# Kernel optimization log

Hardware: AMD Instinct MI355X
Metric: run time of the kernel (lower is better)

## Reference

```python
import jax, jax.numpy as jnp
import numpy as np

B, N, D = 8, 1024, 512
H = 8
DH = D // H
EPS_DIST = 1e-8
EPS_LN = 1e-5


def _layer_norm(x, gamma, beta):
    mu = jnp.mean(x, axis=-1, keepdims=True)
    var = jnp.mean((x - mu) ** 2, axis=-1, keepdims=True)
    return (x - mu) * jax.lax.rsqrt(var + EPS_LN) * gamma + beta


def setup_inputs() -> dict:
    key = jax.random.key(0)
    ks = jax.random.split(key, 6)
    scale = 1.0 / np.sqrt(D)
    inp = {
        "x": jax.random.normal(ks[0], (B, N, D), dtype=jnp.float32),
        "Wq": jax.random.normal(ks[1], (D, D), dtype=jnp.float32) * scale,
        "Wk": jax.random.normal(ks[2], (D, D), dtype=jnp.float32) * scale,
        "Wv": jax.random.normal(ks[3], (D, D), dtype=jnp.float32) * scale,
        "Wo": jax.random.normal(ks[4], (D, D), dtype=jnp.float32) * scale,
        "bq": jnp.zeros((D,), jnp.float32),
        "bk": jnp.zeros((D,), jnp.float32),
        "bv": jnp.zeros((D,), jnp.float32),
        "bo": jnp.zeros((D,), jnp.float32),
        "ln1_g": jnp.ones((D,), jnp.float32),
        "ln1_b": jnp.zeros((D,), jnp.float32),
        "ln2_g": jnp.ones((D,), jnp.float32),
        "ln2_b": jnp.zeros((D,), jnp.float32),
    }
    return inp


def reference(x, Wq, bq, Wk, bk, Wv, bv, Wo, bo, ln1_g, ln1_b, ln2_g, ln2_b):
    residual = x
    h = _layer_norm(x, ln1_g, ln1_b)  # pre-norm

    def heads(t):
        # [B,N,D] -> [B,H,N,DH]
        return t.reshape(B, N, H, DH).transpose(0, 2, 1, 3)

    q = heads(h @ Wq + bq)
    k = heads(h @ Wk + bk)
    v = heads(h @ Wv + bv)

    # Euclidean pairwise distance via ||q||^2 + ||k||^2 - 2 q.k expansion
    q_sq = jnp.sum(q * q, axis=-1)[..., :, None]      # [B,H,N,1]
    k_sq = jnp.sum(k * k, axis=-1)[..., None, :]      # [B,H,1,N]
    qk = jnp.einsum("bhnd,bhmd->bhnm", q, k)          # [B,H,N,N]
    d2 = jnp.maximum(q_sq + k_sq - 2.0 * qk, 0.0)
    dist = jnp.sqrt(d2 + EPS_DIST)

    # distance -> attention score: smaller distance = higher attention
    attn = jax.nn.softmax(-dist, axis=-1)             # [B,H,N,N]

    out = jnp.einsum("bhnm,bhmd->bhnd", attn, v)      # [B,H,N,DH]
    out = out.transpose(0, 2, 1, 3).reshape(B, N, D)
    out = out @ Wo + bo

    y = residual + out
    y = _layer_norm(y, ln2_g, ln2_b)
    return y
```

## Files before the change

kernel.cpp:

```cpp
#include <hip/hip_runtime.h>
#include <math.h>

typedef __attribute__((ext_vector_type(8))) short short8;
typedef __attribute__((ext_vector_type(4))) float f32x4;

constexpr int B  = 8;
constexpr int N  = 1024;
constexpr int D  = 512;
constexpr int H  = 8;
constexpr int DH = 64;
constexpr int M_ROWS = 8192;
constexpr float EPS_DIST = 1e-8f;
constexpr float EPS_LN   = 1e-5f;

__device__ inline unsigned short bfbits(float f) {
    union { float f; unsigned u; } v; v.f = f;
    unsigned r = v.u + 0x7fffu + ((v.u >> 16) & 1u);
    return (unsigned short)(r >> 16);
}
__device__ inline float bf2f(unsigned short s) {
    union { unsigned u; float f; } v; v.u = ((unsigned)s) << 16; return v.f;
}

__device__ inline void async_ld16(unsigned short* lds, const unsigned short* g) {
    __builtin_amdgcn_global_load_lds(
        (const __attribute__((address_space(1))) unsigned int*)(g),
        (__attribute__((address_space(3))) unsigned int*)(lds),
        16, 0, 0);
}

__global__ __launch_bounds__(256) void prep_kernel(const float* __restrict__ Wq,
                                                   const float* __restrict__ Wk,
                                                   const float* __restrict__ Wv,
                                                   const float* __restrict__ Wo,
                                                   unsigned short* __restrict__ WtAll,
                                                   const float* __restrict__ x,
                                                   const float* __restrict__ ln1_g,
                                                   const float* __restrict__ ln1_b,
                                                   unsigned short* __restrict__ h_bf) {
    const int bxg = blockIdx.x;
    if (bxg < 256) {
        int sub = bxg >> 6;
        const float* W = sub == 0 ? Wq : sub == 1 ? Wk : sub == 2 ? Wv : Wo;
        unsigned short* Wt = WtAll + (size_t)sub * 262144;
        int t = (bxg & 63) * 256 + threadIdx.x;
        int tn = t & 127, tk = t >> 7;
        int k = tk * 4, n = tn * 4;
        float4 r0 = *(const float4*)&W[(size_t)(k + 0) * 512 + n];
        float4 r1 = *(const float4*)&W[(size_t)(k + 1) * 512 + n];
        float4 r2 = *(const float4*)&W[(size_t)(k + 2) * 512 + n];
        float4 r3 = *(const float4*)&W[(size_t)(k + 3) * 512 + n];
        ushort4 c;
        c.x = bfbits(r0.x); c.y = bfbits(r1.x); c.z = bfbits(r2.x); c.w = bfbits(r3.x);
        *(ushort4*)&Wt[(size_t)(n + 0) * 512 + k] = c;
        c.x = bfbits(r0.y); c.y = bfbits(r1.y); c.z = bfbits(r2.y); c.w = bfbits(r3.y);
        *(ushort4*)&Wt[(size_t)(n + 1) * 512 + k] = c;
        c.x = bfbits(r0.z); c.y = bfbits(r1.z); c.z = bfbits(r2.z); c.w = bfbits(r3.z);
        *(ushort4*)&Wt[(size_t)(n + 2) * 512 + k] = c;
        c.x = bfbits(r0.w); c.y = bfbits(r1.w); c.z = bfbits(r2.w); c.w = bfbits(r3.w);
        *(ushort4*)&Wt[(size_t)(n + 3) * 512 + k] = c;
    } else {
        const int w = threadIdx.x >> 6, lane = threadIdx.x & 63;
        const int row = (bxg - 256) * 4 + w;
        const float4* xr = (const float4*)(x + (size_t)row * D);
        float4 a = xr[lane], b2 = xr[lane + 64];
        float s = a.x + a.y + a.z + a.w + b2.x + b2.y + b2.z + b2.w;
        #pragma unroll
        for (int o = 1; o < 64; o <<= 1) s += __shfl_xor(s, o, 64);
        const float mu = s * (1.0f / 512.0f);
        float d0 = a.x - mu, d1 = a.y - mu, d2 = a.z - mu, d3 = a.w - mu;
        float e0 = b2.x - mu, e1 = b2.y - mu, e2 = b2.z - mu, e3 = b2.w - mu;
        float vs = d0*d0 + d1*d1 + d2*d2 + d3*d3 + e0*e0 + e1*e1 + e2*e2 + e3*e3;
        #pragma unroll
        for (int o = 1; o < 64; o <<= 1) vs += __shfl_xor(vs, o, 64);
        const float rstd = rsqrtf(vs * (1.0f / 512.0f) + EPS_LN);
        const float4* g4 = (const float4*)ln1_g;
        const float4* b4 = (const float4*)ln1_b;
        float4 ga = g4[lane], gb = g4[lane + 64];
        float4 ba = b4[lane], bb = b4[lane + 64];
        ushort4 u;
        u.x = bfbits(d0 * rstd * ga.x + ba.x);
        u.y = bfbits(d1 * rstd * ga.y + ba.y);
        u.z = bfbits(d2 * rstd * ga.z + ba.z);
        u.w = bfbits(d3 * rstd * ga.w + ba.w);
        *(ushort4*)&h_bf[(size_t)row * 512 + lane * 4] = u;
        u.x = bfbits(e0 * rstd * gb.x + bb.x);
        u.y = bfbits(e1 * rstd * gb.y + bb.y);
        u.z = bfbits(e2 * rstd * gb.z + bb.z);
        u.w = bfbits(e3 * rstd * gb.w + bb.w);
        *(ushort4*)&h_bf[(size_t)row * 512 + 256 + lane * 4] = u;
    }
}

__global__ __launch_bounds__(256) void ln2_kernel(const unsigned short* __restrict__ y0,
                                                  const float* __restrict__ res,
                                                  const float* __restrict__ gamma,
                                                  const float* __restrict__ beta,
                                                  float* __restrict__ out) {
    const int w = threadIdx.x >> 6, lane = threadIdx.x & 63;
    const int row = blockIdx.x * 4 + w;
    const ushort4* y4 = (const ushort4*)(y0 + (size_t)row * D);
    const float4*  r4 = (const float4*)(res + (size_t)row * D);
    ushort4 ya = y4[lane], yb = y4[lane + 64];
    float4  ra = r4[lane], rb = r4[lane + 64];
    float v0 = bf2f(ya.x) + ra.x, v1 = bf2f(ya.y) + ra.y;
    float v2 = bf2f(ya.z) + ra.z, v3 = bf2f(ya.w) + ra.w;
    float v4 = bf2f(yb.x) + rb.x, v5 = bf2f(yb.y) + rb.y;
    float v6 = bf2f(yb.z) + rb.z, v7 = bf2f(yb.w) + rb.w;
    float s = v0 + v1 + v2 + v3 + v4 + v5 + v6 + v7;
    #pragma unroll
    for (int o = 1; o < 64; o <<= 1) s += __shfl_xor(s, o, 64);
    const float mu = s * (1.0f / 512.0f);
    v0 -= mu; v1 -= mu; v2 -= mu; v3 -= mu;
    v4 -= mu; v5 -= mu; v6 -= mu; v7 -= mu;
    float vs = v0*v0 + v1*v1 + v2*v2 + v3*v3 + v4*v4 + v5*v5 + v6*v6 + v7*v7;
    #pragma unroll
    for (int o = 1; o < 64; o <<= 1) vs += __shfl_xor(vs, o, 64);
    const float rstd = rsqrtf(vs * (1.0f / 512.0f) + EPS_LN);
    const float4* g4 = (const float4*)gamma;
    const float4* b4 = (const float4*)beta;
    float4 ga = g4[lane], gb = g4[lane + 64];
    float4 ba = b4[lane], bb = b4[lane + 64];
    float4 o1, o2;
    o1.x = v0 * rstd * ga.x + ba.x; o1.y = v1 * rstd * ga.y + ba.y;
    o1.z = v2 * rstd * ga.z + ba.z; o1.w = v3 * rstd * ga.w + ba.w;
    o2.x = v4 * rstd * gb.x + bb.x; o2.y = v5 * rstd * gb.y + bb.y;
    o2.z = v6 * rstd * gb.z + bb.z; o2.w = v7 * rstd * gb.w + bb.w;
    float4* orow = (float4*)(out + (size_t)row * D);
    orow[lane]      = o1;
    orow[lane + 64] = o2;
}

template <int MODE, int MT>
__global__ __launch_bounds__(256) void gemm128(const unsigned short* __restrict__ A,
                                               const unsigned short* __restrict__ Wt,
                                               const float* __restrict__ bias0,
                                               const float* __restrict__ bias1,
                                               const float* __restrict__ bias2,
                                               void* __restrict__ o0,
                                               unsigned short* __restrict__ Ko,
                                               unsigned short* __restrict__ Vo,
                                               float* __restrict__ sq0,
                                               float* __restrict__ sq1) {
    constexpr int RB = M_ROWS / MT;
    constexpr int NI = MT / 32;
    constexpr int ASZ = MT * 64, BSZ = 128 * 64;
    constexpr int SMSZ = (MODE == 1) ? ((ASZ + BSZ > 18432) ? ASZ + BSZ : 18432)
                                     : (ASZ + BSZ);
    __shared__ unsigned short smem[SMSZ];
    unsigned short* As = smem;
    unsigned short* Bs = smem + ASZ;

    const int id = blockIdx.x;
    const int by = id & (RB - 1), bx = id / RB;
    const int tid = threadIdx.x;
    const int lane = tid & 63, wv = tid >> 6;
    const int quad = lane >> 4, l15 = lane & 15;
    const int row0 = by * MT, col0 = bx * 128;
    const int wm = (wv & 1) * (MT / 2), wn = (wv >> 1) * 64;

    f32x4 acc[NI][4];
    #pragma unroll
    for (int i = 0; i < NI; ++i)
        #pragma unroll
        for (int j = 0; j < 4; ++j) acc[i][j] = (f32x4){0.f, 0.f, 0.f, 0.f};

    const unsigned short* Ag = A  + (size_t)row0 * 512;
    const unsigned short* Bg = Wt + (size_t)col0 * 512;

    for (int k0 = 0; k0 < 512; k0 += 64) {
        __syncthreads();
        #pragma unroll
        for (int c = 0; c < ASZ / 2048; ++c) {
            int fu = c * 2048 + tid * 8;
            int r = fu >> 6, ko = fu & 63;
            async_ld16(As + fu, Ag + (size_t)r * 512 + k0 + ko);
        }
        #pragma unroll
        for (int c = 0; c < BSZ / 2048; ++c) {
            int fu = c * 2048 + tid * 8;
            int r = fu >> 6, ko = fu & 63;
            async_ld16(Bs + fu, Bg + (size_t)r * 512 + k0 + ko);
        }
        __syncthreads();

        #pragma unroll
        for (int ks = 0; ks < 2; ++ks) {
            short8 af[NI], bf[4];
            #pragma unroll
            for (int i = 0; i < NI; ++i)
                af[i] = *(const short8*)&As[(wm + i * 16 + l15) * 64 + ks * 32 + quad * 8];
            #pragma unroll
            for (int j = 0; j < 4; ++j)
                bf[j] = *(const short8*)&Bs[(wn + j * 16 + l15) * 64 + ks * 32 + quad * 8];
            #pragma unroll
            for (int i = 0; i < NI; ++i)
                #pragma unroll
                for (int j = 0; j < 4; ++j)
                    acc[i][j] = __builtin_amdgcn_mfma_f32_16x16x32_bf16(af[i], bf[j], acc[i][j], 0, 0, 0);
        }
    }

    if (MODE == 0) {
        unsigned short* C = (unsigned short*)o0;
        #pragma unroll
        for (int i = 0; i < NI; ++i)
            #pragma unroll
            for (int j = 0; j < 4; ++j) {
                int col = col0 + wn + j * 16 + l15;
                float bv = bias0[col];
                #pragma unroll
                for (int r = 0; r < 4; ++r) {
                    int row = row0 + wm + i * 16 + quad * 4 + r;
                    C[(size_t)row * 512 + col] = bfbits(acc[i][j][r] + bv);
                }
            }
    } else {
        const int colg = col0 + wn;
        const int seg = colg >> 9;
        const int hh = (colg & 511) >> 6;
        const float* bias = seg == 0 ? bias0 : seg == 1 ? bias1 : bias2;

        if (seg < 2) {
            unsigned short* dst = seg == 0 ? (unsigned short*)o0 : Ko;
            float* sq = seg == 0 ? sq0 : sq1;
            #pragma unroll
            for (int i = 0; i < NI; ++i) {
                const int m0 = row0 + wm + i * 16 + quad * 4;
                float ss[4] = {0.f, 0.f, 0.f, 0.f};
                #pragma unroll
                for (int j = 0; j < 4; ++j) {
                    float bvj = bias[hh * 64 + j * 16 + l15];
                    #pragma unroll
                    for (int r = 0; r < 4; ++r) {
                        float v = acc[i][j][r] + bvj;
                        unsigned short ub = bfbits(v);
                        float vr = bf2f(ub);
                        ss[r] += vr * vr;
                        int m = m0 + r;
                        int b_ = m >> 10, n_ = m & 1023;
                        dst[((size_t)((b_ * 8 + hh) * 1024) + n_) * 64 + j * 16 + l15] = ub;
                    }
                }
                #pragma unroll
                for (int r = 0; r < 4; ++r) {
                    float s = ss[r];
                    s += __shfl_xor(s, 1, 64);
                    s += __shfl_xor(s, 2, 64);
                    s += __shfl_xor(s, 4, 64);
                    s += __shfl_xor(s, 8, 64);
                    if (l15 == 0) {
                        int m = m0 + r;
                        sq[(size_t)((m >> 10) * 8 + hh) * 1024 + (m & 1023)] = s;
                    }
                }
            }
        } else {
            __syncthreads();
            unsigned short* T = smem + wv * 4608;
            #pragma unroll
            for (int i = 0; i < NI; ++i)
                #pragma unroll
                for (int j = 0; j < 4; ++j) {
                    float bvj = bias[hh * 64 + j * 16 + l15];
                    ushort4 pk;
                    pk.x = bfbits(acc[i][j][0] + bvj);
                    pk.y = bfbits(acc[i][j][1] + bvj);
                    pk.z = bfbits(acc[i][j][2] + bvj);
                    pk.w = bfbits(acc[i][j][3] + bvj);
                    *(ushort4*)&T[(j * 16 + l15) * 72 + i * 16 + quad * 4] = pk;
                }
            const int b_ = (row0 + wm) >> 10;
            const int nbase = (row0 + wm) & 1023;
            unsigned short* Vg = Vo + ((size_t)((b_ * 8 + hh) * 64)) * 1024 + nbase;
            #pragma unroll
            for (int it = 0; it < 8; ++it) {
                int dl = it * 8 + (lane >> 3);
                int nl = (lane & 7) * 8;
                uint4 v = *(const uint4*)&T[dl * 72 + nl];
                *(uint4*)&Vg[(size_t)dl * 1024 + nl] = v;
            }
        }
    }
}

__global__ __launch_bounds__(256) void attn_kernel(const unsigned short* __restrict__ Q,
                                                   const unsigned short* __restrict__ K,
                                                   const unsigned short* __restrict__ Vt,
                                                   const float* __restrict__ qsq,
                                                   const float* __restrict__ ksq,
                                                   unsigned short* __restrict__ O) {
    __shared__ unsigned short Ks[2][64][72];
    __shared__ unsigned short Vs[2][64][72];
    __shared__ unsigned short Ps[4][32][72];
    __shared__ float ksq_s[2][64];

    const int id = blockIdx.x;
    const int bh = id & 63, qb = id >> 6;
    const int q0 = qb * 128;
    const int tid = threadIdx.x;
    const int lane = tid & 63, w = tid >> 6;
    const int quad = lane >> 4, l15 = lane & 15;
    const int b_ = bh >> 3, h_ = bh & 7;

    const unsigned short* Qb = Q  + (size_t)bh * N * DH;
    const unsigned short* Kb = K  + (size_t)bh * N * DH;
    const unsigned short* Vb = Vt + (size_t)bh * DH * N;

    short8 qf[2][2];
    #pragma unroll
    for (int qh = 0; qh < 2; ++qh) {
        const unsigned short* qp = Qb + (size_t)(q0 + w * 32 + qh * 16 + l15) * 64 + quad * 8;
        qf[qh][0] = *(const short8*)qp;
        qf[qh][1] = *(const short8*)(qp + 32);
    }
    float qe[2][4];
    #pragma unroll
    for (int qh = 0; qh < 2; ++qh)
        #pragma unroll
        for (int r = 0; r < 4; ++r)
            qe[qh][r] = qsq[bh * N + q0 + w * 32 + qh * 16 + quad * 4 + r] + EPS_DIST;

    f32x4 oacc[2][4];
    #pragma unroll
    for (int qh = 0; qh < 2; ++qh)
        #pragma unroll
        for (int dt = 0; dt < 4; ++dt) oacc[qh][dt] = (f32x4){0.f, 0.f, 0.f, 0.f};
    float dpart[2][4] = {};

    const int e0 = tid, e1 = tid + 256;
    const int r0s = e0 >> 3, c0s = (e0 & 7) * 8;
    const int r1s = e1 >> 3, c1s = (e1 & 7) * 8;
    uint4 kreg0, kreg1, vreg0, vreg1;
    float ksreg = 0.f;

    kreg0 = *(const uint4*)(Kb + (size_t)r0s * 64 + c0s);
    kreg1 = *(const uint4*)(Kb + (size_t)r1s * 64 + c1s);
    vreg0 = *(const uint4*)(Vb + (size_t)r0s * N + c0s);
    vreg1 = *(const uint4*)(Vb + (size_t)r1s * N + c1s);
    if (tid < 64) ksreg = ksq[bh * N + tid];

    *(uint4*)&Ks[0][r0s][c0s] = kreg0;
    *(uint4*)&Ks[0][r1s][c1s] = kreg1;
    *(uint4*)&Vs[0][r0s][c0s] = vreg0;
    *(uint4*)&Vs[0][r1s][c1s] = vreg1;
    if (tid < 64) ksq_s[0][tid] = ksreg;
    __syncthreads();

    for (int kt = 0; kt < 16; ++kt) {
        const int cur = kt & 1;
        if (kt < 15) {
            kreg0 = *(const uint4*)(Kb + (size_t)((kt + 1) * 64 + r0s) * 64 + c0s);
            kreg1 = *(const uint4*)(Kb + (size_t)((kt + 1) * 64 + r1s) * 64 + c1s);
            vreg0 = *(const uint4*)(Vb + (size_t)r0s * N + (kt + 1) * 64 + c0s);
            vreg1 = *(const uint4*)(Vb + (size_t)r1s * N + (kt + 1) * 64 + c1s);
            if (tid < 64) ksreg = ksq[bh * N + (kt + 1) * 64 + tid];
        }

        #pragma unroll
        for (int kb = 0; kb < 4; ++kb) {
            short8 kf0 = *(const short8*)&Ks[cur][kb * 16 + l15][quad * 8];
            short8 kf1 = *(const short8*)&Ks[cur][kb * 16 + l15][32 + quad * 8];
            float ks2 = ksq_s[cur][kb * 16 + l15];
            #pragma unroll
            for (int qh = 0; qh < 2; ++qh) {
                f32x4 sa = (f32x4){0.f, 0.f, 0.f, 0.f};
                sa = __builtin_amdgcn_mfma_f32_16x16x32_bf16(qf[qh][0], kf0, sa, 0, 0, 0);
                sa = __builtin_amdgcn_mfma_f32_16x16x32_bf16(qf[qh][1], kf1, sa, 0, 0, 0);
                #pragma unroll
                for (int r = 0; r < 4; ++r) {
                    float d2 = fmaf(-2.0f, sa[r], qe[qh][r] + ks2);
                    d2 = fmaxf(d2, EPS_DIST);
                    float p = __expf(-__builtin_amdgcn_sqrtf(d2));
                    dpart[qh][r] += p;
                    union { float f; unsigned u; } pu; pu.f = p;
                    Ps[w][qh * 16 + quad * 4 + r][kb * 16 + l15] = (unsigned short)(pu.u >> 16);
                }
            }
        }

        short8 vf[4][2];
        #pragma unroll
        for (int dt = 0; dt < 4; ++dt)
            #pragma unroll
            for (int kc = 0; kc < 2; ++kc)
                vf[dt][kc] = *(const short8*)&Vs[cur][dt * 16 + l15][kc * 32 + quad * 8];
        #pragma unroll
        for (int kc = 0; kc < 2; ++kc) {
            short8 pf0 = *(const short8*)&Ps[w][l15][kc * 32 + quad * 8];
            short8 pf1 = *(const short8*)&Ps[w][16 + l15][kc * 32 + quad * 8];
            #pragma unroll
            for (int dt = 0; dt < 4; ++dt) {
                oacc[0][dt] = __builtin_amdgcn_mfma_f32_16x16x32_bf16(pf0, vf[dt][kc], oacc[0][dt], 0, 0, 0);
                oacc[1][dt] = __builtin_amdgcn_mfma_f32_16x16x32_bf16(pf1, vf[dt][kc], oacc[1][dt], 0, 0, 0);
            }
        }

        if (kt < 15) {
            *(uint4*)&Ks[cur ^ 1][r0s][c0s] = kreg0;
            *(uint4*)&Ks[cur ^ 1][r1s][c1s] = kreg1;
            *(uint4*)&Vs[cur ^ 1][r0s][c0s] = vreg0;
            *(uint4*)&Vs[cur ^ 1][r1s][c1s] = vreg1;
            if (tid < 64) ksq_s[cur ^ 1][tid] = ksreg;
        }
        __syncthreads();
    }

    float rinv[2][4];
    #pragma unroll
    for (int qh = 0; qh < 2; ++qh)
        #pragma unroll
        for (int r = 0; r < 4; ++r) {
            float s = dpart[qh][r];
            s += __shfl_xor(s, 1, 64);
            s += __shfl_xor(s, 2, 64);
            s += __shfl_xor(s, 4, 64);
            s += __shfl_xor(s, 8, 64);
            rinv[qh][r] = __builtin_amdgcn_rcpf(s);
        }

    #pragma unroll
    for (int qh = 0; qh < 2; ++qh)
        #pragma unroll
        for (int dt = 0; dt < 4; ++dt)
            #pragma unroll
            for (int r = 0; r < 4; ++r) {
                int n_ = q0 + w * 32 + qh * 16 + quad * 4 + r;
                O[((size_t)(b_ * N + n_) * D) + h_ * DH + dt * 16 + l15] =
                    bfbits(oacc[qh][dt][r] * rinv[qh][r]);
            }
}

extern "C" void kernel_launch(void* const* d_in, const int* in_sizes, int n_in,
                              void* d_out, int out_size, void* d_ws, size_t ws_size,
                              hipStream_t stream) {
    const float* x     = (const float*)d_in[0];
    const float* Wq    = (const float*)d_in[1];
    const float* Wk    = (const float*)d_in[2];
    const float* Wv    = (const float*)d_in[3];
    const float* Wo    = (const float*)d_in[4];
    const float* bq    = (const float*)d_in[5];
    const float* bk    = (const float*)d_in[6];
    const float* bv    = (const float*)d_in[7];
    const float* bo    = (const float*)d_in[8];
    const float* ln1_g = (const float*)d_in[9];
    const float* ln1_b = (const float*)d_in[10];
    const float* ln2_g = (const float*)d_in[11];
    const float* ln2_b = (const float*)d_in[12];
    float* out = (float*)d_out;

    unsigned short* WtAll = (unsigned short*)d_ws;
    unsigned short* h_bf  = WtAll + 4 * 262144;
    unsigned short* Qb    = h_bf + 4194304;
    unsigned short* Kb    = Qb + 4194304;
    unsigned short* Vtg   = Kb + 4194304;
    unsigned short* Ob    = Vtg + 4194304;
    unsigned short* Y0    = Ob + 4194304;
    float* qsq = (float*)(Y0 + 4194304);
    float* ksq = qsq + 65536;

    prep_kernel<<<256 + M_ROWS / 4, 256, 0, stream>>>(Wq, Wk, Wv, Wo, WtAll,
                                                      x, ln1_g, ln1_b, h_bf);

    gemm128<1, 128><<<768, 256, 0, stream>>>(h_bf, WtAll, bq, bk, bv,
                                             Qb, Kb, Vtg, qsq, ksq);

    attn_kernel<<<512, 256, 0, stream>>>(Qb, Kb, Vtg, qsq, ksq, Ob);

    gemm128<0, 64><<<512, 256, 0, stream>>>(Ob, WtAll + 3 * 262144, bo,
                                            nullptr, nullptr, Y0,
                                            nullptr, nullptr, nullptr, nullptr);

    ln2_kernel<<<M_ROWS / 4, 256, 0, stream>>>(Y0, x, ln2_g, ln2_b, out);
}
```

Baseline: 180.1 us.

## Keep attention probabilities in registers via permlane swaps and swizzle K/V LDS tiles

The attention kernel now computes the transposed score tile, with K as the A operand. Q fragments are pre-scaled by -2 through a bf16 bit trick, and the accumulator is seeded with ||q||^2+||k||^2, so the distance expansion folds into the MFMA. The bf16 probabilities are packed and redistributed across lanes with permlane32/permlane16 swaps. This replaces the round trip through the per-wave Ps LDS buffer and feeds the PV MFMAs directly. K/V LDS tiles drop their padding in favour of an XOR swizzle, and row normalizers are broadcast through a small LDS scratch. The change removes LDS traffic and bank conflicts, at the cost of more lane-permute work and a bit-hack scaling that treats zero and subnormal inputs slightly differently.

```diff
diff --git a/kernel.cpp b/kernel.cpp
--- a/kernel.cpp
+++ b/kernel.cpp
@@ -3,6 +3,7 @@
 
 typedef __attribute__((ext_vector_type(8))) short short8;
 typedef __attribute__((ext_vector_type(4))) float f32x4;
+typedef __attribute__((ext_vector_type(2))) unsigned uint2v;
 
 constexpr int B  = 8;
 constexpr int N  = 1024;
@@ -290,9 +291,8 @@
                                                    const float* __restrict__ qsq,
                                                    const float* __restrict__ ksq,
                                                    unsigned short* __restrict__ O) {
-    __shared__ unsigned short Ks[2][64][72];
-    __shared__ unsigned short Vs[2][64][72];
-    __shared__ unsigned short Ps[4][32][72];
+    __shared__ unsigned short Ks[2][64][64];
+    __shared__ unsigned short Vs[2][64][64];
     __shared__ float ksq_s[2][64];
 
     const int id = blockIdx.x;
@@ -313,111 +313,132 @@
         const unsigned short* qp = Qb + (size_t)(q0 + w * 32 + qh * 16 + l15) * 64 + quad * 8;
         qf[qh][0] = *(const short8*)qp;
         qf[qh][1] = *(const short8*)(qp + 32);
-    }
-    float qe[2][4];
+        unsigned* qw = (unsigned*)&qf[qh][0];
+        #pragma unroll
+        for (int j = 0; j < 8; ++j) qw[j] = (qw[j] ^ 0x80008000u) + 0x00800080u;
+    }
+    float qe[2];
+    qe[0] = qsq[bh * N + q0 + w * 32 + l15] + EPS_DIST;
+    qe[1] = qsq[bh * N + q0 + w * 32 + 16 + l15] + EPS_DIST;
+
+    f32x4 oacc[2][4];
     #pragma unroll
     for (int qh = 0; qh < 2; ++qh)
         #pragma unroll
-        for (int r = 0; r < 4; ++r)
-            qe[qh][r] = qsq[bh * N + q0 + w * 32 + qh * 16 + quad * 4 + r] + EPS_DIST;
-
-    f32x4 oacc[2][4];
-    #pragma unroll
-    for (int qh = 0; qh < 2; ++qh)
-        #pragma unroll
         for (int dt = 0; dt < 4; ++dt) oacc[qh][dt] = (f32x4){0.f, 0.f, 0.f, 0.f};
-    float dpart[2][4] = {};
-
-    const int e0 = tid, e1 = tid + 256;
-    const int r0s = e0 >> 3, c0s = (e0 & 7) * 8;
-    const int r1s = e1 >> 3, c1s = (e1 & 7) * 8;
+    float dsum[2] = {0.f, 0.f};
+
+    const int r0s = tid >> 3, r1s = r0s + 32;
+    const int cbase = (tid & 7) * 8;
+    const int csw = cbase ^ ((r0s & 7) << 3);
     uint4 kreg0, kreg1, vreg0, vreg1;
     float ksreg = 0.f;
 
-    kreg0 = *(const uint4*)(Kb + (size_t)r0s * 64 + c0s);
-    kreg1 = *(const uint4*)(Kb + (size_t)r1s * 64 + c1s);
-    vreg0 = *(const uint4*)(Vb + (size_t)r0s * N + c0s);
-    vreg1 = *(const uint4*)(Vb + (size_t)r1s * N + c1s);
+    kreg0 = *(const uint4*)(Kb + (size_t)r0s * 64 + cbase);
+    kreg1 = *(const uint4*)(Kb + (size_t)r1s * 64 + cbase);
+    vreg0 = *(const uint4*)(Vb + (size_t)r0s * N + cbase);
+    vreg1 = *(const uint4*)(Vb + (size_t)r1s * N + cbase);
     if (tid < 64) ksreg = ksq[bh * N + tid];
 
-    *(uint4*)&Ks[0][r0s][c0s] = kreg0;
-    *(uint4*)&Ks[0][r1s][c1s] = kreg1;
-    *(uint4*)&Vs[0][r0s][c0s] = vreg0;
-    *(uint4*)&Vs[0][r1s][c1s] = vreg1;
+    *(uint4*)&Ks[0][r0s][csw] = kreg0;
+    *(uint4*)&Ks[0][r1s][csw] = kreg1;
+    *(uint4*)&Vs[0][r0s][csw] = vreg0;
+    *(uint4*)&Vs[0][r1s][csw] = vreg1;
     if (tid < 64) ksq_s[0][tid] = ksreg;
     __syncthreads();
 
     for (int kt = 0; kt < 16; ++kt) {
         const int cur = kt & 1;
         if (kt < 15) {
-            kreg0 = *(const uint4*)(Kb + (size_t)((kt + 1) * 64 + r0s) * 64 + c0s);
-            kreg1 = *(const uint4*)(Kb + (size_t)((kt + 1) * 64 + r1s) * 64 + c1s);
-            vreg0 = *(const uint4*)(Vb + (size_t)r0s * N + (kt + 1) * 64 + c0s);
-            vreg1 = *(const uint4*)(Vb + (size_t)r1s * N + (kt + 1) * 64 + c1s);
+            kreg0 = *(const uint4*)(Kb + (size_t)((kt + 1) * 64 + r0s) * 64 + cbase);
+            kreg1 = *(const uint4*)(Kb + (size_t)((kt + 1) * 64 + r1s) * 64 + cbase);
+            vreg0 = *(const uint4*)(Vb + (size_t)r0s * N + (kt + 1) * 64 + cbase);
+            vreg1 = *(const uint4*)(Vb + (size_t)r1s * N + (kt + 1) * 64 + cbase);
             if (tid < 64) ksreg = ksq[bh * N + (kt + 1) * 64 + tid];
         }
 
         #pragma unroll
-        for (int kb = 0; kb < 4; ++kb) {
-            short8 kf0 = *(const short8*)&Ks[cur][kb * 16 + l15][quad * 8];
-            short8 kf1 = *(const short8*)&Ks[cur][kb * 16 + l15][32 + quad * 8];
-            float ks2 = ksq_s[cur][kb * 16 + l15];
+        for (int kc = 0; kc < 2; ++kc) {
+            unsigned Wp[2][2][2];
+            #pragma unroll
+            for (int kh = 0; kh < 2; ++kh) {
+                const int kb = kc * 2 + kh;
+                const int krow = kb * 16 + l15;
+                const int ksw = (krow & 7) << 3;
+                short8 kf0 = *(const short8*)&Ks[cur][krow][(quad * 8) ^ ksw];
+                short8 kf1 = *(const short8*)&Ks[cur][krow][(32 + quad * 8) ^ ksw];
+                f32x4 ks2 = *(const f32x4*)&ksq_s[cur][kb * 16 + quad * 4];
+                #pragma unroll
+                for (int qh = 0; qh < 2; ++qh) {
+                    f32x4 sa;
+                    #pragma unroll
+                    for (int r = 0; r < 4; ++r) sa[r] = ks2[r] + qe[qh];
+                    sa = __builtin_amdgcn_mfma_f32_16x16x32_bf16(kf0, qf[qh][0], sa, 0, 0, 0);
+                    sa = __builtin_amdgcn_mfma_f32_16x16x32_bf16(kf1, qf[qh][1], sa, 0, 0, 0);
+                    float pr[4];
+                    #pragma unroll
+                    for (int r = 0; r < 4; ++r) {
+                        float d2 = fmaxf(sa[r], EPS_DIST);
+                        float p = __expf(-__builtin_amdgcn_sqrtf(d2));
+                        dsum[qh] += p;
+                        pr[r] = p;
+                    }
+                    union { float f; unsigned u; } u0, u1, u2, u3;
+                    u0.f = pr[0]; u1.f = pr[1]; u2.f = pr[2]; u3.f = pr[3];
+                    Wp[qh][kh][0] = (u1.u & 0xFFFF0000u) | (u0.u >> 16);
+                    Wp[qh][kh][1] = (u3.u & 0xFFFF0000u) | (u2.u >> 16);
+                }
+            }
+
+            short8 vf[4];
+            #pragma unroll
+            for (int dt = 0; dt < 4; ++dt) {
+                const int vrow = dt * 16 + l15;
+                vf[dt] = *(const short8*)&Vs[cur][vrow][(kc * 32 + quad * 8) ^ ((vrow & 7) << 3)];
+            }
+
             #pragma unroll
             for (int qh = 0; qh < 2; ++qh) {
-                f32x4 sa = (f32x4){0.f, 0.f, 0.f, 0.f};
-                sa = __builtin_amdgcn_mfma_f32_16x16x32_bf16(qf[qh][0], kf0, sa, 0, 0, 0);
-                sa = __builtin_amdgcn_mfma_f32_16x16x32_bf16(qf[qh][1], kf1, sa, 0, 0, 0);
-                #pragma unroll
-                for (int r = 0; r < 4; ++r) {
-                    float d2 = fmaf(-2.0f, sa[r], qe[qh][r] + ks2);
-                    d2 = fmaxf(d2, EPS_DIST);
-                    float p = __expf(-__builtin_amdgcn_sqrtf(d2));
-                    dpart[qh][r] += p;
-                    union { float f; unsigned u; } pu; pu.f = p;
-                    Ps[w][qh * 16 + quad * 4 + r][kb * 16 + l15] = (unsigned short)(pu.u >> 16);
-                }
-            }
-        }
-
-        short8 vf[4][2];
-        #pragma unroll
-        for (int dt = 0; dt < 4; ++dt)
-            #pragma unroll
-            for (int kc = 0; kc < 2; ++kc)
-                vf[dt][kc] = *(const short8*)&Vs[cur][dt * 16 + l15][kc * 32 + quad * 8];
-        #pragma unroll
-        for (int kc = 0; kc < 2; ++kc) {
-            short8 pf0 = *(const short8*)&Ps[w][l15][kc * 32 + quad * 8];
-            short8 pf1 = *(const short8*)&Ps[w][16 + l15][kc * 32 + quad * 8];
-            #pragma unroll
-            for (int dt = 0; dt < 4; ++dt) {
-                oacc[0][dt] = __builtin_amdgcn_mfma_f32_16x16x32_bf16(pf0, vf[dt][kc], oacc[0][dt], 0, 0, 0);
-                oacc[1][dt] = __builtin_amdgcn_mfma_f32_16x16x32_bf16(pf1, vf[dt][kc], oacc[1][dt], 0, 0, 0);
+                uint2v ya = __builtin_amdgcn_permlane32_swap(Wp[qh][0][0], Wp[qh][1][0], false, false);
+                uint2v za = __builtin_amdgcn_permlane16_swap(ya.x, ya.y, false, false);
+                uint2v yb = __builtin_amdgcn_permlane32_swap(Wp[qh][0][1], Wp[qh][1][1], false, false);
+                uint2v zb = __builtin_amdgcn_permlane16_swap(yb.x, yb.y, false, false);
+                union { unsigned wds[4]; short8 s; } pu;
+                pu.wds[0] = za.x; pu.wds[1] = zb.x; pu.wds[2] = za.y; pu.wds[3] = zb.y;
+                short8 pf = pu.s;
+                #pragma unroll
+                for (int dt = 0; dt < 4; ++dt)
+                    oacc[qh][dt] = __builtin_amdgcn_mfma_f32_16x16x32_bf16(pf, vf[dt], oacc[qh][dt], 0, 0, 0);
             }
         }
 
         if (kt < 15) {
-            *(uint4*)&Ks[cur ^ 1][r0s][c0s] = kreg0;
-            *(uint4*)&Ks[cur ^ 1][r1s][c1s] = kreg1;
-            *(uint4*)&Vs[cur ^ 1][r0s][c0s] = vreg0;
-            *(uint4*)&Vs[cur ^ 1][r1s][c1s] = vreg1;
+            *(uint4*)&Ks[cur ^ 1][r0s][csw] = kreg0;
+            *(uint4*)&Ks[cur ^ 1][r1s][csw] = kreg1;
+            *(uint4*)&Vs[cur ^ 1][r0s][csw] = vreg0;
+            *(uint4*)&Vs[cur ^ 1][r1s][csw] = vreg1;
             if (tid < 64) ksq_s[cur ^ 1][tid] = ksreg;
         }
         __syncthreads();
     }
 
-    float rinv[2][4];
-    #pragma unroll
-    for (int qh = 0; qh < 2; ++qh)
-        #pragma unroll
-        for (int r = 0; r < 4; ++r) {
-            float s = dpart[qh][r];
-            s += __shfl_xor(s, 1, 64);
-            s += __shfl_xor(s, 2, 64);
-            s += __shfl_xor(s, 4, 64);
-            s += __shfl_xor(s, 8, 64);
-            rinv[qh][r] = __builtin_amdgcn_rcpf(s);
-        }
+    float rinv[2];
+    #pragma unroll
+    for (int qh = 0; qh < 2; ++qh) {
+        float s = dsum[qh];
+        s += __shfl_xor(s, 16, 64);
+        s += __shfl_xor(s, 32, 64);
+        rinv[qh] = __builtin_amdgcn_rcpf(s);
+    }
+
+    float* sc = (float*)ksq_s;
+    if (lane < 16) {
+        sc[w * 32 + l15]      = rinv[0];
+        sc[w * 32 + 16 + l15] = rinv[1];
+    }
+    f32x4 rv[2];
+    rv[0] = *(const f32x4*)&sc[w * 32 + quad * 4];
+    rv[1] = *(const f32x4*)&sc[w * 32 + 16 + quad * 4];
 
     #pragma unroll
     for (int qh = 0; qh < 2; ++qh)
@@ -427,7 +448,7 @@
             for (int r = 0; r < 4; ++r) {
                 int n_ = q0 + w * 32 + qh * 16 + quad * 4 + r;
                 O[((size_t)(b_ * N + n_) * D) + h_ * DH + dt * 16 + l15] =
-                    bfbits(oacc[qh][dt][r] * rinv[qh][r]);
+                    bfbits(oacc[qh][dt][r] * rv[qh][r]);
             }
 }
 
```

Result: no change. 180.8 us (+0.4%).
